# Optimization experiments

Hardware: AMD Instinct MI355X
Metric: run time of the kernel (lower is better)

## Reference

```python
import jax, jax.numpy as jnp
import numpy as np

N_GRAPHS = 20000
N_NODES = 7          # nodes per NAS cell
HID = 256            # hidden_dim
N_OPS = 5
TAU = 1.0


def _glorot(key, shape):
    s = 1.0 / np.sqrt(shape[0])
    return jax.random.normal(key, shape, jnp.float32) * s


def setup_inputs() -> dict:
    key = jax.random.key(0)
    ks = jax.random.split(key, 12)
    N = N_GRAPHS * N_NODES
    # fully-connected DAG edges inside each graph (upper triangular, 21 per graph)
    sl, dl = np.triu_indices(N_NODES, k=1)
    offs = (np.arange(N_GRAPHS) * N_NODES)[:, None]
    src = (offs + sl[None, :]).reshape(-1)
    dst = (offs + dl[None, :]).reshape(-1)
    edge_index = jnp.asarray(np.stack([src, dst]), dtype=jnp.int32)  # [2, E]
    batch = jnp.asarray(np.repeat(np.arange(N_GRAPHS), N_NODES), dtype=jnp.int32)
    E = edge_index.shape[1]
    return {
        "x": jax.random.normal(ks[0], (N, HID), jnp.float32),
        "edge_index": edge_index,
        "batch": batch,
        "W1": _glorot(ks[1], (HID, HID)), "b1": jnp.zeros((HID,), jnp.float32),
        "W2": _glorot(ks[2], (HID, HID)), "b2": jnp.zeros((HID,), jnp.float32),
        "We": _glorot(ks[3], (2 * HID, 2)), "be": jnp.zeros((2,), jnp.float32),
        "Wm": _glorot(ks[4], (HID, N_OPS)), "bm": jnp.zeros((N_OPS,), jnp.float32),
        "g_edge": jax.random.gumbel(ks[5], (E, 2), jnp.float32),
        "g_op": jax.random.gumbel(ks[6], (N, N_OPS), jnp.float32),
    }


def gcn_conv(x, edge_index, W, b, edge_weight=None):
    """PyG-style GCNConv: add self-loops (weight 1), symmetric normalization."""
    N = x.shape[0]
    src, dst = edge_index[0], edge_index[1]
    E = src.shape[0]
    ew = jnp.ones((E,), x.dtype) if edge_weight is None else edge_weight
    loop = jnp.arange(N, dtype=src.dtype)
    src_a = jnp.concatenate([src, loop])
    dst_a = jnp.concatenate([dst, loop])
    ew_a = jnp.concatenate([ew, jnp.ones((N,), x.dtype)])
    deg = jax.ops.segment_sum(ew_a, dst_a, num_segments=N)
    dinv = jnp.where(deg > 0, jax.lax.rsqrt(jnp.maximum(deg, 1e-12)), 0.0)
    norm = dinv[src_a] * ew_a * dinv[dst_a]  # [E+N]
    h = x @ W  # [N, out]
    msg = norm[:, None] * h[src_a]
    return jax.ops.segment_sum(msg, dst_a, num_segments=N) + b


def gumbel_softmax(logits, g, tau, hard):
    y = jax.nn.softmax((logits + g) / tau, axis=-1)
    if hard:
        y_hard = jax.nn.one_hot(jnp.argmax(y, axis=-1), y.shape[-1], dtype=y.dtype)
        y = y_hard + y - jax.lax.stop_gradient(y)
    return y


def reference(x, edge_index, batch, W1, b1, W2, b2, We, be, Wm, bm, g_edge, g_op):
    # mu=2 GCN layers with ReLU
    h = jax.nn.relu(gcn_conv(x, edge_index, W1, b1))
    h = jax.nn.relu(gcn_conv(h, edge_index, W2, b2))
    # edge scorer: 2-way gumbel-softmax over (keep, drop) per edge
    src, dst = edge_index[0], edge_index[1]
    pair = jnp.concatenate([h[src], h[dst]], axis=-1)  # [E, 2*HID]
    edge_logits = pair @ We + be                       # [E, 2]
    edges_scores = gumbel_softmax(edge_logits, g_edge, TAU, hard=False)
    # sample_pre=False branch: average the two score channels as edge weight
    avg_scores = (edges_scores[:, 0] + edges_scores[:, 1]) / 2
    op_emb = gcn_conv(h, edge_index, Wm, bm, edge_weight=avg_scores)  # [N, N_OPS]
    # hard straight-through gumbel-softmax over operations
    op_indices = gumbel_softmax(op_emb, g_op, TAU, hard=True)
    return op_indices
```

## Files before the change

kernel.cpp:

```cpp
#include <hip/hip_runtime.h>
#include <math.h>

#define HID 256

typedef __attribute__((ext_vector_type(8))) short v8s;
typedef __attribute__((ext_vector_type(4))) float v4f;

__device__ __forceinline__ float d1c(int i){ return 1.0f/sqrtf((float)(i+1)); }
__device__ __forceinline__ float d2c(int i){ return 1.0f/sqrtf(1.0f+0.5f*(float)i); }

__device__ __forceinline__ unsigned short f2bf(float x){
    unsigned u = __float_as_uint(x);
    u += 0x7fffu + ((u>>16)&1u);
    return (unsigned short)(u>>16);
}
__device__ __forceinline__ float bf2f(unsigned short b){
    return __uint_as_float(((unsigned)b)<<16);
}

__device__ __forceinline__ void mixA1_2(float (&v)[7][2]) {
#pragma unroll
    for (int r = 6; r >= 0; --r) {
        float t0 = 0.f, t1 = 0.f;
#pragma unroll
        for (int i = 0; i <= r; ++i) {
            const float c = d1c(i) * d1c(r);
            t0 = fmaf(c, v[i][0], t0);
            t1 = fmaf(c, v[i][1], t1);
        }
        v[r][0] = t0; v[r][1] = t1;
    }
}

__global__ void prep_w(const float* __restrict__ W1, const float* __restrict__ W2,
                       unsigned short* __restrict__ outw)
{
    const int tid = blockIdx.x*256 + threadIdx.x;
    if (tid >= 2*3*8*16*64) return;
    const int l  = tid & 63;
    const int c  = tid >> 6;
    const int nt = c & 15;
    const int k0 = (c>>4) & 7;
    const int s  = (c>>7) % 3;
    const int L  = c / (3*8*16);
    const float* W = L ? W2 : W1;
    const int n = nt*16 + (l & 15);
    unsigned short* o = outw + (size_t)tid*8;
#pragma unroll
    for (int e = 0; e < 8; ++e){
        const int k = k0*32 + (l>>4)*8 + e;
        float x = W[k*HID + n];
        unsigned short b0 = f2bf(x); float rr = x - bf2f(b0);
        unsigned short b1 = f2bf(rr); rr -= bf2f(b1);
        unsigned short b2 = f2bf(rr);
        o[e] = (s==0)? b0 : (s==1)? b1 : b2;
    }
}

__global__ __launch_bounds__(256, 2)
void nas_mfma(const float* __restrict__ X,
              const float* __restrict__ b1, const float* __restrict__ b2,
              const float* __restrict__ Wm, const float* __restrict__ bm,
              const float* __restrict__ g_op,
              const unsigned short* __restrict__ Bw,
              float* __restrict__ out)
{
    __shared__ __align__(16) char smem[49152];
    char*  Q0  = smem;
    char*  Q1  = smem + 24576;
    float* bq0 = (float*)smem;
    float* bq1 = (float*)(smem + 24576);
    float* bnc = (float*)smem;

    const int t   = threadIdx.x;
    const int w   = t >> 6;
    const int l   = t & 63;
    const int l15 = l & 15;
    const int q   = l >> 4;
    const int g   = t >> 5;
    const int t31 = t & 31;
    const long node0 = (long)blockIdx.x * 56;

    auto ws_q = [&](const float (&v)[7][2], char* qb){
        const int slotbase = t31 >> 2;
        const int byteoff  = (t31 & 3) * 4;
#pragma unroll
        for (int r = 0; r < 7; ++r){
            const int row  = g*7 + r;
            const int slot = slotbase ^ (row & 7);
            char* p = qb + row*128 + slot*16 + byteoff;
            unsigned h0[2], h1[2], h2[2];
#pragma unroll
            for (int j = 0; j < 2; ++j){
                float x = v[r][j];
                unsigned short a = f2bf(x); float rr = x - bf2f(a);
                unsigned short b = f2bf(rr); rr -= bf2f(b);
                unsigned short c = f2bf(rr);
                h0[j] = a; h1[j] = b; h2[j] = c;
            }
            *(unsigned*)(p)         = h0[0] | (h0[1] << 16);
            *(unsigned*)(p + 8192)  = h1[0] | (h1[1] << 16);
            *(unsigned*)(p + 16384) = h2[0] | (h2[1] << 16);
        }
    };

    auto gemm_q = [&](v4f (&ac)[4][4], const unsigned short* lbase, int qi,
                      const char* qb){
        const unsigned short* bbase = lbase + (size_t)w*512 + (size_t)l*8;
        v8s Bb[3][4];
        auto loadB = [&](int gi, int buf){
            const int ksl = gi/3, s2 = gi%3;
            const unsigned short* bp = bbase + (size_t)((s2*8 + qi*2 + ksl)*16)*512;
            Bb[buf][0] = *(const v8s*)(bp);
            Bb[buf][1] = *(const v8s*)(bp + 2048);
            Bb[buf][2] = *(const v8s*)(bp + 4096);
            Bb[buf][3] = *(const v8s*)(bp + 6144);
        };
        loadB(0, 0);
        loadB(1, 1);
        v8s A[3][4];
#pragma unroll
        for (int gi = 0; gi < 6; ++gi){
            const int ksl = gi/3, s2 = gi%3;
            if (s2 == 0){
                const int xorslot = ((ksl*4 + q) ^ (l15 & 7)) << 4;
#pragma unroll
                for (int s = 0; s < 3; ++s)
#pragma unroll
                for (int mt = 0; mt < 4; ++mt)
                    A[s][mt] = *(const v8s*)(qb + s*8192 + (mt*16 + l15)*128 + xorslot);
            }
            if (gi + 2 < 6) loadB(gi + 2, (gi + 2) % 3);
            const int buf = gi % 3;
            __builtin_amdgcn_s_setprio(1);
#pragma unroll
            for (int s1 = 0; s1 < 3; ++s1){
                if (s1 + s2 > 2) continue;
#pragma unroll
                for (int mt = 0; mt < 4; ++mt){
                    ac[mt][0] = __builtin_amdgcn_mfma_f32_16x16x32_bf16(A[s1][mt], Bb[buf][0], ac[mt][0],0,0,0);
                    ac[mt][1] = __builtin_amdgcn_mfma_f32_16x16x32_bf16(A[s1][mt], Bb[buf][1], ac[mt][1],0,0,0);
                    ac[mt][2] = __builtin_amdgcn_mfma_f32_16x16x32_bf16(A[s1][mt], Bb[buf][2], ac[mt][2],0,0,0);
                    ac[mt][3] = __builtin_amdgcn_mfma_f32_16x16x32_bf16(A[s1][mt], Bb[buf][3], ac[mt][3],0,0,0);
                }
            }
            __builtin_amdgcn_s_setprio(0);
        }
    };

    auto bw_q = [&](const v4f (&ac)[4][4], int p, float* bq){
        const int cc = (w*16 + l15) ^ (q << 4);
#pragma unroll
        for (int mt = 0; mt < 4; ++mt)
#pragma unroll
        for (int j = 0; j < 4; ++j)
            bq[(mt*16 + q*4 + j)*64 + cc] = ac[mt][p][j];
    };
    auto rd_q = [&](float (&v)[7][2], const float* bq){
#pragma unroll
        for (int r = 0; r < 7; ++r){
            const int row = g*7 + r;
            const int sw  = ((row >> 2) & 3) << 4;
            float2 f = *(const float2*)(&bq[row*64 + ((2*t31) ^ sw)]);
            v[r][0] = f.x; v[r][1] = f.y;
        }
    };
    auto brm = [&](float (&v)[7][2], const float* bias, int p){
        float2 bb = *(const float2*)(bias + p*64 + 2*t31);
#pragma unroll
        for (int r = 0; r < 7; ++r){
            v[r][0] = fmaxf(v[r][0] + bb.x, 0.0f);
            v[r][1] = fmaxf(v[r][1] + bb.y, 0.0f);
        }
        mixA1_2(v);
    };

    v4f acc[4][4];
#pragma unroll
    for (int mt=0;mt<4;++mt)
#pragma unroll
    for (int p=0;p<4;++p) acc[mt][p] = (v4f){0.f,0.f,0.f,0.f};

    float xq[4][7][2];
    {
        const float* xp = X + (node0 + g*7)*HID + 2*t31;
#pragma unroll
        for (int r = 0; r < 7; ++r)
#pragma unroll
        for (int qq = 0; qq < 4; ++qq){
            float2 f = *(const float2*)(xp + (long)r*HID + qq*64);
            xq[qq][r][0] = f.x; xq[qq][r][1] = f.y;
        }
#pragma unroll
        for (int qq = 0; qq < 4; ++qq) mixA1_2(xq[qq]);
    }

    ws_q(xq[0], Q0);
    __syncthreads();
    ws_q(xq[1], Q1); gemm_q(acc, Bw, 0, Q0);
    __syncthreads();
    ws_q(xq[2], Q0); gemm_q(acc, Bw, 1, Q1);
    __syncthreads();
    ws_q(xq[3], Q1); gemm_q(acc, Bw, 2, Q0);
    __syncthreads();
    gemm_q(acc, Bw, 3, Q1); bw_q(acc, 0, bq0);
    __syncthreads();

    v4f acc2[4][4];
#pragma unroll
    for (int mt=0;mt<4;++mt)
#pragma unroll
    for (int p=0;p<4;++p) acc2[mt][p] = (v4f){0.f,0.f,0.f,0.f};
    const unsigned short* Bw2 = Bw + 196608;

    float v0[7][2], v1[7][2];
    rd_q(v0, bq0); bw_q(acc, 1, bq1);
    __syncthreads();
    brm(v0, b1, 0); ws_q(v0, Q0); rd_q(v1, bq1);
    __syncthreads();
    brm(v1, b1, 1); ws_q(v1, Q1); gemm_q(acc2, Bw2, 0, Q0);
    __syncthreads();
    bw_q(acc, 2, bq0); gemm_q(acc2, Bw2, 1, Q1);
    __syncthreads();
    rd_q(v0, bq0); bw_q(acc, 3, bq1);
    __syncthreads();
    brm(v0, b1, 2); ws_q(v0, Q0); rd_q(v1, bq1);
    __syncthreads();
    brm(v1, b1, 3); ws_q(v1, Q1); gemm_q(acc2, Bw2, 2, Q0);
    __syncthreads();
    gemm_q(acc2, Bw2, 3, Q1);
    __syncthreads();

    auto bw2 = [&](const v4f (&ac)[4][4], int h){
#pragma unroll
        for (int pb = 0; pb < 2; ++pb){
            const int p  = 2*h + pb;
            const int lc = (w + 4*pb)*16 + l15;
            const int sw = ((q&1)<<4) ^ ((q>>1)<<2);
#pragma unroll
            for (int mt = 0; mt < 4; ++mt)
#pragma unroll
            for (int j = 0; j < 4; ++j){
                const int row = mt*16 + q*4 + j;
                bnc[row*128 + (lc ^ sw)] = ac[mt][p][j];
            }
        }
    };

    float pm[7][5];
#pragma unroll
    for (int r=0;r<7;++r)
#pragma unroll
    for (int p=0;p<5;++p) pm[r][p] = 0.0f;

    auto stage_pm = [&](int h){
        float v[7][4];
        const int lc = 4*t31;
#pragma unroll
        for (int r = 0; r < 7; ++r){
            const int row = g*7 + r;
            const int qq  = (row>>2)&3;
            const int sw  = ((qq&1)<<4) ^ ((qq>>1)<<2);
            float4 f = *(const float4*)(&bnc[row*128 + (lc ^ sw)]);
            v[r][0]=f.x; v[r][1]=f.y; v[r][2]=f.z; v[r][3]=f.w;
        }
        float4 bb = *(const float4*)(b2 + h*128 + 4*t31);
        const float bia[4] = {bb.x, bb.y, bb.z, bb.w};
#pragma unroll
        for (int r = 0; r < 7; ++r)
#pragma unroll
        for (int j = 0; j < 4; ++j)
            v[r][j] = fmaxf(v[r][j] + bia[j], 0.0f);
        const int colg = h*128 + 4*t31;
#pragma unroll
        for (int j = 0; j < 4; ++j){
            const float* wr = Wm + (colg + j)*5;
            float w5[5];
#pragma unroll
            for (int p = 0; p < 5; ++p) w5[p] = wr[p];
#pragma unroll
            for (int r = 0; r < 7; ++r)
#pragma unroll
            for (int p = 0; p < 5; ++p)
                pm[r][p] = fmaf(v[r][j], w5[p], pm[r][p]);
        }
    };

    bw2(acc2, 0);
    __syncthreads();
    stage_pm(0);
    __syncthreads();
    bw2(acc2, 1);
    __syncthreads();
    stage_pm(1);

#pragma unroll
    for (int m = 16; m >= 1; m >>= 1)
#pragma unroll
        for (int r = 0; r < 7; ++r)
#pragma unroll
            for (int p = 0; p < 5; ++p)
                pm[r][p] += __shfl_xor(pm[r][p], m, 64);

    if (t31 < 7){
        const int rr = t31;
        const long node = node0 + g*7 + rr;
        const float d2r = d2c(rr);
        float op[5];
#pragma unroll
        for (int p = 0; p < 5; ++p) op[p] = bm[p];
#pragma unroll
        for (int i = 0; i < 7; ++i){
            const float wgt = (i > rr) ? 0.0f
                            : (((i < rr) ? 0.5f : 1.0f) * d2c(i) * d2r);
#pragma unroll
            for (int p = 0; p < 5; ++p)
                op[p] = fmaf(wgt, pm[i][p], op[p]);
        }
        const float* gp = g_op + node*5;
        float best = op[0] + gp[0];
        int bi = 0;
#pragma unroll
        for (int p = 1; p < 5; ++p){
            float u = op[p] + gp[p];
            if (u > best) { best = u; bi = p; }
        }
        float* o = out + node*5;
#pragma unroll
        for (int p = 0; p < 5; ++p) o[p] = (p == bi) ? 1.0f : 0.0f;
    }
}

extern "C" void kernel_launch(void* const* d_in, const int* in_sizes, int n_in,
                              void* d_out, int out_size, void* d_ws, size_t ws_size,
                              hipStream_t stream)
{
    const float* X   = (const float*)d_in[0];
    const float* W1  = (const float*)d_in[3];
    const float* b1  = (const float*)d_in[4];
    const float* W2  = (const float*)d_in[5];
    const float* b2  = (const float*)d_in[6];
    const float* Wm  = (const float*)d_in[9];
    const float* bm  = (const float*)d_in[10];
    const float* gop = (const float*)d_in[12];
    float* out = (float*)d_out;

    unsigned short* wsplit = (unsigned short*)d_ws;

    prep_w<<<192, 256, 0, stream>>>(W1, W2, wsplit);

    const int N       = in_sizes[0] / HID;
    const int ngraph  = N / 7;
    const int nblocks = ngraph / 8;

    nas_mfma<<<nblocks, 256, 0, stream>>>(X, b1, b2, Wm, bm, gop, wsplit, out);
}
```

Before: 403.9 us.

## Halve per-block tile to 4 graphs to raise occupancy and cut registers

```diff
diff --git a/kernel.cpp b/kernel.cpp
--- a/kernel.cpp
+++ b/kernel.cpp
@@ -16,20 +16,6 @@
 }
 __device__ __forceinline__ float bf2f(unsigned short b){
     return __uint_as_float(((unsigned)b)<<16);
-}
-
-__device__ __forceinline__ void mixA1_2(float (&v)[7][2]) {
-#pragma unroll
-    for (int r = 6; r >= 0; --r) {
-        float t0 = 0.f, t1 = 0.f;
-#pragma unroll
-        for (int i = 0; i <= r; ++i) {
-            const float c = d1c(i) * d1c(r);
-            t0 = fmaf(c, v[i][0], t0);
-            t1 = fmaf(c, v[i][1], t1);
-        }
-        v[r][0] = t0; v[r][1] = t1;
-    }
 }
 
 __global__ void prep_w(const float* __restrict__ W1, const float* __restrict__ W2,
@@ -57,7 +43,7 @@
     }
 }
 
-__global__ __launch_bounds__(256, 2)
+__global__ __launch_bounds__(256, 3)
 void nas_mfma(const float* __restrict__ X,
               const float* __restrict__ b1, const float* __restrict__ b2,
               const float* __restrict__ Wm, const float* __restrict__ bm,
@@ -65,49 +51,41 @@
               const unsigned short* __restrict__ Bw,
               float* __restrict__ out)
 {
-    __shared__ __align__(16) char smem[49152];
+    __shared__ __align__(16) char smem[24576];
     char*  Q0  = smem;
-    char*  Q1  = smem + 24576;
+    char*  Q1  = smem + 12288;
     float* bq0 = (float*)smem;
-    float* bq1 = (float*)(smem + 24576);
-    float* bnc = (float*)smem;
+    float* bq1 = (float*)(smem + 12288);
 
     const int t   = threadIdx.x;
     const int w   = t >> 6;
     const int l   = t & 63;
     const int l15 = l & 15;
     const int q   = l >> 4;
-    const int g   = t >> 5;
-    const int t31 = t & 31;
-    const long node0 = (long)blockIdx.x * 56;
-
-    auto ws_q = [&](const float (&v)[7][2], char* qb){
-        const int slotbase = t31 >> 2;
-        const int byteoff  = (t31 & 3) * 4;
+    const long node0 = (long)blockIdx.x * 28;
+
+    auto ws_q = [&](const float (&v)[7], char* qb){
+        const int slotpre = l >> 3;
+        const int byteoff = (l & 7) * 2;
 #pragma unroll
         for (int r = 0; r < 7; ++r){
-            const int row  = g*7 + r;
-            const int slot = slotbase ^ (row & 7);
+            const int row  = w*7 + r;
+            const int slot = slotpre ^ (row & 7);
             char* p = qb + row*128 + slot*16 + byteoff;
-            unsigned h0[2], h1[2], h2[2];
-#pragma unroll
-            for (int j = 0; j < 2; ++j){
-                float x = v[r][j];
-                unsigned short a = f2bf(x); float rr = x - bf2f(a);
-                unsigned short b = f2bf(rr); rr -= bf2f(b);
-                unsigned short c = f2bf(rr);
-                h0[j] = a; h1[j] = b; h2[j] = c;
-            }
-            *(unsigned*)(p)         = h0[0] | (h0[1] << 16);
-            *(unsigned*)(p + 8192)  = h1[0] | (h1[1] << 16);
-            *(unsigned*)(p + 16384) = h2[0] | (h2[1] << 16);
-        }
-    };
-
-    auto gemm_q = [&](v4f (&ac)[4][4], const unsigned short* lbase, int qi,
+            float x = v[r];
+            unsigned short a = f2bf(x); float rr = x - bf2f(a);
+            unsigned short b = f2bf(rr); rr -= bf2f(b);
+            unsigned short c = f2bf(rr);
+            *(unsigned short*)(p)        = a;
+            *(unsigned short*)(p + 4096) = b;
+            *(unsigned short*)(p + 8192) = c;
+        }
+    };
+
+    auto gemm_q = [&](v4f (&ac)[2][4], const unsigned short* lbase, int qi,
                       const char* qb){
         const unsigned short* bbase = lbase + (size_t)w*512 + (size_t)l*8;
-        v8s Bb[3][4];
+        v8s Bb[2][4];
         auto loadB = [&](int gi, int buf){
             const int ksl = gi/3, s2 = gi%3;
             const unsigned short* bp = bbase + (size_t)((s2*8 + qi*2 + ksl)*16)*512;
@@ -117,8 +95,7 @@
             Bb[buf][3] = *(const v8s*)(bp + 6144);
         };
         loadB(0, 0);
-        loadB(1, 1);
-        v8s A[3][4];
+        v8s A[3][2];
 #pragma unroll
         for (int gi = 0; gi < 6; ++gi){
             const int ksl = gi/3, s2 = gi%3;
@@ -127,17 +104,17 @@
 #pragma unroll
                 for (int s = 0; s < 3; ++s)
 #pragma unroll
-                for (int mt = 0; mt < 4; ++mt)
-                    A[s][mt] = *(const v8s*)(qb + s*8192 + (mt*16 + l15)*128 + xorslot);
+                for (int mt = 0; mt < 2; ++mt)
+                    A[s][mt] = *(const v8s*)(qb + s*4096 + (mt*16 + l15)*128 + xorslot);
             }
-            if (gi + 2 < 6) loadB(gi + 2, (gi + 2) % 3);
-            const int buf = gi % 3;
+            if (gi + 1 < 6) loadB(gi + 1, (gi + 1) & 1);
+            const int buf = gi & 1;
             __builtin_amdgcn_s_setprio(1);
 #pragma unroll
             for (int s1 = 0; s1 < 3; ++s1){
                 if (s1 + s2 > 2) continue;
 #pragma unroll
-                for (int mt = 0; mt < 4; ++mt){
+                for (int mt = 0; mt < 2; ++mt){
                     ac[mt][0] = __builtin_amdgcn_mfma_f32_16x16x32_bf16(A[s1][mt], Bb[buf][0], ac[mt][0],0,0,0);
                     ac[mt][1] = __builtin_amdgcn_mfma_f32_16x16x32_bf16(A[s1][mt], Bb[buf][1], ac[mt][1],0,0,0);
                     ac[mt][2] = __builtin_amdgcn_mfma_f32_16x16x32_bf16(A[s1][mt], Bb[buf][2], ac[mt][2],0,0,0);
@@ -148,104 +125,85 @@
         }
     };
 
-    auto bw_q = [&](const v4f (&ac)[4][4], int p, float* bq){
+    auto bw_q = [&](const v4f (&ac)[2][4], int p, float* bq){
         const int cc = (w*16 + l15) ^ (q << 4);
 #pragma unroll
-        for (int mt = 0; mt < 4; ++mt)
+        for (int mt = 0; mt < 2; ++mt)
 #pragma unroll
         for (int j = 0; j < 4; ++j)
             bq[(mt*16 + q*4 + j)*64 + cc] = ac[mt][p][j];
     };
-    auto rd_q = [&](float (&v)[7][2], const float* bq){
+    auto rd_s = [&](float (&v)[7], const float* bq){
 #pragma unroll
         for (int r = 0; r < 7; ++r){
-            const int row = g*7 + r;
+            const int row = w*7 + r;
             const int sw  = ((row >> 2) & 3) << 4;
-            float2 f = *(const float2*)(&bq[row*64 + ((2*t31) ^ sw)]);
-            v[r][0] = f.x; v[r][1] = f.y;
-        }
-    };
-    auto brm = [&](float (&v)[7][2], const float* bias, int p){
-        float2 bb = *(const float2*)(bias + p*64 + 2*t31);
-#pragma unroll
-        for (int r = 0; r < 7; ++r){
-            v[r][0] = fmaxf(v[r][0] + bb.x, 0.0f);
-            v[r][1] = fmaxf(v[r][1] + bb.y, 0.0f);
-        }
-        mixA1_2(v);
-    };
-
-    v4f acc[4][4];
-#pragma unroll
-    for (int mt=0;mt<4;++mt)
+            v[r] = bq[row*64 + (l ^ sw)];
+        }
+    };
+    auto mix7 = [&](float (&v)[7]){
+#pragma unroll
+        for (int r = 6; r >= 0; --r){
+            float tt = 0.f;
+#pragma unroll
+            for (int i = 0; i <= r; ++i) tt = fmaf(d1c(i)*d1c(r), v[i], tt);
+            v[r] = tt;
+        }
+    };
+    auto brm = [&](float (&v)[7], const float* bias, int p){
+        const float bb = bias[p*64 + l];
+#pragma unroll
+        for (int r = 0; r < 7; ++r) v[r] = fmaxf(v[r] + bb, 0.0f);
+        mix7(v);
+    };
+    auto ldx = [&](float (&v)[7], int qq){
+        const float* xp = X + (node0 + w*7)*HID + qq*64 + l;
+#pragma unroll
+        for (int r = 0; r < 7; ++r) v[r] = xp[(long)r*HID];
+    };
+
+    v4f acc[2][4];
+#pragma unroll
+    for (int mt=0;mt<2;++mt)
 #pragma unroll
     for (int p=0;p<4;++p) acc[mt][p] = (v4f){0.f,0.f,0.f,0.f};
 
-    float xq[4][7][2];
-    {
-        const float* xp = X + (node0 + g*7)*HID + 2*t31;
-#pragma unroll
-        for (int r = 0; r < 7; ++r)
-#pragma unroll
-        for (int qq = 0; qq < 4; ++qq){
-            float2 f = *(const float2*)(xp + (long)r*HID + qq*64);
-            xq[qq][r][0] = f.x; xq[qq][r][1] = f.y;
-        }
-#pragma unroll
-        for (int qq = 0; qq < 4; ++qq) mixA1_2(xq[qq]);
-    }
-
-    ws_q(xq[0], Q0);
-    __syncthreads();
-    ws_q(xq[1], Q1); gemm_q(acc, Bw, 0, Q0);
-    __syncthreads();
-    ws_q(xq[2], Q0); gemm_q(acc, Bw, 1, Q1);
-    __syncthreads();
-    ws_q(xq[3], Q1); gemm_q(acc, Bw, 2, Q0);
+    float va[7], vb[7];
+    ldx(va, 0); mix7(va); ws_q(va, Q0);
+    ldx(vb, 1); mix7(vb);
+    __syncthreads();
+    ws_q(vb, Q1); ldx(va, 2); mix7(va); gemm_q(acc, Bw, 0, Q0);
+    __syncthreads();
+    ws_q(va, Q0); ldx(vb, 3); mix7(vb); gemm_q(acc, Bw, 1, Q1);
+    __syncthreads();
+    ws_q(vb, Q1); gemm_q(acc, Bw, 2, Q0);
     __syncthreads();
     gemm_q(acc, Bw, 3, Q1); bw_q(acc, 0, bq0);
     __syncthreads();
 
-    v4f acc2[4][4];
-#pragma unroll
-    for (int mt=0;mt<4;++mt)
+    v4f acc2[2][4];
+#pragma unroll
+    for (int mt=0;mt<2;++mt)
 #pragma unroll
     for (int p=0;p<4;++p) acc2[mt][p] = (v4f){0.f,0.f,0.f,0.f};
     const unsigned short* Bw2 = Bw + 196608;
 
-    float v0[7][2], v1[7][2];
-    rd_q(v0, bq0); bw_q(acc, 1, bq1);
-    __syncthreads();
-    brm(v0, b1, 0); ws_q(v0, Q0); rd_q(v1, bq1);
-    __syncthreads();
-    brm(v1, b1, 1); ws_q(v1, Q1); gemm_q(acc2, Bw2, 0, Q0);
+    rd_s(va, bq0); bw_q(acc, 1, bq1);
+    __syncthreads();
+    brm(va, b1, 0); ws_q(va, Q0); rd_s(vb, bq1);
+    __syncthreads();
+    brm(vb, b1, 1); ws_q(vb, Q1); gemm_q(acc2, Bw2, 0, Q0);
     __syncthreads();
     bw_q(acc, 2, bq0); gemm_q(acc2, Bw2, 1, Q1);
     __syncthreads();
-    rd_q(v0, bq0); bw_q(acc, 3, bq1);
-    __syncthreads();
-    brm(v0, b1, 2); ws_q(v0, Q0); rd_q(v1, bq1);
-    __syncthreads();
-    brm(v1, b1, 3); ws_q(v1, Q1); gemm_q(acc2, Bw2, 2, Q0);
-    __syncthreads();
-    gemm_q(acc2, Bw2, 3, Q1);
-    __syncthreads();
-
-    auto bw2 = [&](const v4f (&ac)[4][4], int h){
-#pragma unroll
-        for (int pb = 0; pb < 2; ++pb){
-            const int p  = 2*h + pb;
-            const int lc = (w + 4*pb)*16 + l15;
-            const int sw = ((q&1)<<4) ^ ((q>>1)<<2);
-#pragma unroll
-            for (int mt = 0; mt < 4; ++mt)
-#pragma unroll
-            for (int j = 0; j < 4; ++j){
-                const int row = mt*16 + q*4 + j;
-                bnc[row*128 + (lc ^ sw)] = ac[mt][p][j];
-            }
-        }
-    };
+    rd_s(va, bq0); bw_q(acc, 3, bq1);
+    __syncthreads();
+    brm(va, b1, 2); ws_q(va, Q0); rd_s(vb, bq1);
+    __syncthreads();
+    brm(vb, b1, 3); ws_q(vb, Q1); gemm_q(acc2, Bw2, 2, Q0);
+    __syncthreads();
+    gemm_q(acc2, Bw2, 3, Q1); bw_q(acc2, 0, bq0);
+    __syncthreads();
 
     float pm[7][5];
 #pragma unroll
@@ -253,58 +211,42 @@
 #pragma unroll
     for (int p=0;p<5;++p) pm[r][p] = 0.0f;
 
-    auto stage_pm = [&](int h){
-        float v[7][4];
-        const int lc = 4*t31;
-#pragma unroll
-        for (int r = 0; r < 7; ++r){
-            const int row = g*7 + r;
-            const int qq  = (row>>2)&3;
-            const int sw  = ((qq&1)<<4) ^ ((qq>>1)<<2);
-            float4 f = *(const float4*)(&bnc[row*128 + (lc ^ sw)]);
-            v[r][0]=f.x; v[r][1]=f.y; v[r][2]=f.z; v[r][3]=f.w;
-        }
-        float4 bb = *(const float4*)(b2 + h*128 + 4*t31);
-        const float bia[4] = {bb.x, bb.y, bb.z, bb.w};
+    auto pm_q = [&](int p, const float* bq){
+        float v[7];
+        rd_s(v, bq);
+        const float bb = b2[p*64 + l];
+#pragma unroll
+        for (int r = 0; r < 7; ++r) v[r] = fmaxf(v[r] + bb, 0.0f);
+        const float* wr = Wm + (p*64 + l)*5;
+        float w5[5];
+#pragma unroll
+        for (int j = 0; j < 5; ++j) w5[j] = wr[j];
 #pragma unroll
         for (int r = 0; r < 7; ++r)
 #pragma unroll
-        for (int j = 0; j < 4; ++j)
-            v[r][j] = fmaxf(v[r][j] + bia[j], 0.0f);
-        const int colg = h*128 + 4*t31;
-#pragma unroll
-        for (int j = 0; j < 4; ++j){
-            const float* wr = Wm + (colg + j)*5;
-            float w5[5];
-#pragma unroll
-            for (int p = 0; p < 5; ++p) w5[p] = wr[p];
-#pragma unroll
-            for (int r = 0; r < 7; ++r)
-#pragma unroll
-            for (int p = 0; p < 5; ++p)
-                pm[r][p] = fmaf(v[r][j], w5[p], pm[r][p]);
-        }
-    };
-
-    bw2(acc2, 0);
-    __syncthreads();
-    stage_pm(0);
-    __syncthreads();
-    bw2(acc2, 1);
-    __syncthreads();
-    stage_pm(1);
-
-#pragma unroll
-    for (int m = 16; m >= 1; m >>= 1)
+        for (int j = 0; j < 5; ++j)
+            pm[r][j] = fmaf(v[r], w5[j], pm[r][j]);
+    };
+
+    pm_q(0, bq0); bw_q(acc2, 1, bq1);
+    __syncthreads();
+    pm_q(1, bq1); bw_q(acc2, 2, bq0);
+    __syncthreads();
+    pm_q(2, bq0); bw_q(acc2, 3, bq1);
+    __syncthreads();
+    pm_q(3, bq1);
+
+#pragma unroll
+    for (int m = 32; m >= 1; m >>= 1)
 #pragma unroll
         for (int r = 0; r < 7; ++r)
 #pragma unroll
             for (int p = 0; p < 5; ++p)
                 pm[r][p] += __shfl_xor(pm[r][p], m, 64);
 
-    if (t31 < 7){
-        const int rr = t31;
-        const long node = node0 + g*7 + rr;
+    if (l < 7){
+        const int rr = l;
+        const long node = node0 + w*7 + rr;
         const float d2r = d2c(rr);
         float op[5];
 #pragma unroll
@@ -351,7 +293,6 @@
 
     const int N       = in_sizes[0] / HID;
     const int ngraph  = N / 7;
-    const int nblocks = ngraph / 8;
-
+    const int nblocks = ngraph / 4;
     nas_mfma<<<nblocks, 256, 0, stream>>>(X, b1, b2, Wm, bm, gop, wsplit, out);
 }
```

Measured after the change: 421.4 us. 4.3% more time.

## Single-buffer LDS staging and cut registers to fit three blocks per CU

Applied to the files above, without the earlier changes.

```diff
diff --git a/kernel.cpp b/kernel.cpp
--- a/kernel.cpp
+++ b/kernel.cpp
@@ -57,7 +57,7 @@
     }
 }
 
-__global__ __launch_bounds__(256, 2)
+__global__ __launch_bounds__(256, 3)
 void nas_mfma(const float* __restrict__ X,
               const float* __restrict__ b1, const float* __restrict__ b2,
               const float* __restrict__ Wm, const float* __restrict__ bm,
@@ -65,12 +65,9 @@
               const unsigned short* __restrict__ Bw,
               float* __restrict__ out)
 {
-    __shared__ __align__(16) char smem[49152];
-    char*  Q0  = smem;
-    char*  Q1  = smem + 24576;
-    float* bq0 = (float*)smem;
-    float* bq1 = (float*)(smem + 24576);
-    float* bnc = (float*)smem;
+    __shared__ __align__(16) char smem[24576 + 16384];
+    char*  Q  = smem;
+    float* bq = (float*)(smem + 24576);
 
     const int t   = threadIdx.x;
     const int w   = t >> 6;
@@ -81,33 +78,35 @@
     const int t31 = t & 31;
     const long node0 = (long)blockIdx.x * 56;
 
-    auto ws_q = [&](const float (&v)[7][2], char* qb){
-        const int slotbase = t31 >> 2;
-        const int byteoff  = (t31 & 3) * 4;
+    auto split2 = [&](float x, float y, unsigned &u0, unsigned &u1, unsigned &u2){
+        asm("v_cvt_pk_bf16_f32 %0, %1, %2" : "=v"(u0) : "v"(x), "v"(y));
+        float rx = x - __uint_as_float(u0 << 16);
+        float ry = y - __uint_as_float(u0 & 0xffff0000u);
+        asm("v_cvt_pk_bf16_f32 %0, %1, %2" : "=v"(u1) : "v"(rx), "v"(ry));
+        rx -= __uint_as_float(u1 << 16);
+        ry -= __uint_as_float(u1 & 0xffff0000u);
+        asm("v_cvt_pk_bf16_f32 %0, %1, %2" : "=v"(u2) : "v"(rx), "v"(ry));
+    };
+
+    auto ws_q = [&](const float (&v)[7][2]){
+        const int hs      = t31 >> 2;
+        const int byteoff = (t31 & 3) * 4;
 #pragma unroll
         for (int r = 0; r < 7; ++r){
             const int row  = g*7 + r;
-            const int slot = slotbase ^ (row & 7);
-            char* p = qb + row*128 + slot*16 + byteoff;
-            unsigned h0[2], h1[2], h2[2];
-#pragma unroll
-            for (int j = 0; j < 2; ++j){
-                float x = v[r][j];
-                unsigned short a = f2bf(x); float rr = x - bf2f(a);
-                unsigned short b = f2bf(rr); rr -= bf2f(b);
-                unsigned short c = f2bf(rr);
-                h0[j] = a; h1[j] = b; h2[j] = c;
-            }
-            *(unsigned*)(p)         = h0[0] | (h0[1] << 16);
-            *(unsigned*)(p + 8192)  = h1[0] | (h1[1] << 16);
-            *(unsigned*)(p + 16384) = h2[0] | (h2[1] << 16);
-        }
-    };
-
-    auto gemm_q = [&](v4f (&ac)[4][4], const unsigned short* lbase, int qi,
-                      const char* qb){
+            const int slot = hs ^ (row & 7);
+            char* p = Q + row*128 + slot*16 + byteoff;
+            unsigned u0, u1, u2;
+            split2(v[r][0], v[r][1], u0, u1, u2);
+            *(unsigned*)(p)         = u0;
+            *(unsigned*)(p + 8192)  = u1;
+            *(unsigned*)(p + 16384) = u2;
+        }
+    };
+
+    auto gemm_q = [&](v4f (&ac)[4][4], const unsigned short* lbase, int qi){
         const unsigned short* bbase = lbase + (size_t)w*512 + (size_t)l*8;
-        v8s Bb[3][4];
+        v8s Bb[2][4];
         auto loadB = [&](int gi, int buf){
             const int ksl = gi/3, s2 = gi%3;
             const unsigned short* bp = bbase + (size_t)((s2*8 + qi*2 + ksl)*16)*512;
@@ -117,21 +116,20 @@
             Bb[buf][3] = *(const v8s*)(bp + 6144);
         };
         loadB(0, 0);
-        loadB(1, 1);
         v8s A[3][4];
 #pragma unroll
         for (int gi = 0; gi < 6; ++gi){
             const int ksl = gi/3, s2 = gi%3;
             if (s2 == 0){
-                const int xorslot = ((ksl*4 + q) ^ (l15 & 7)) << 4;
+                const int xorslot = ((ksl*4 + q) ^ (l & 7)) << 4;
 #pragma unroll
                 for (int s = 0; s < 3; ++s)
 #pragma unroll
                 for (int mt = 0; mt < 4; ++mt)
-                    A[s][mt] = *(const v8s*)(qb + s*8192 + (mt*16 + l15)*128 + xorslot);
+                    A[s][mt] = *(const v8s*)(Q + s*8192 + (mt*16 + l15)*128 + xorslot);
             }
-            if (gi + 2 < 6) loadB(gi + 2, (gi + 2) % 3);
-            const int buf = gi % 3;
+            if (gi + 1 < 6) loadB(gi + 1, (gi + 1) & 1);
+            const int buf = gi & 1;
             __builtin_amdgcn_s_setprio(1);
 #pragma unroll
             for (int s1 = 0; s1 < 3; ++s1){
@@ -148,7 +146,7 @@
         }
     };
 
-    auto bw_q = [&](const v4f (&ac)[4][4], int p, float* bq){
+    auto bw_q = [&](const v4f (&ac)[4][4], int p){
         const int cc = (w*16 + l15) ^ (q << 4);
 #pragma unroll
         for (int mt = 0; mt < 4; ++mt)
@@ -156,7 +154,7 @@
         for (int j = 0; j < 4; ++j)
             bq[(mt*16 + q*4 + j)*64 + cc] = ac[mt][p][j];
     };
-    auto rd_q = [&](float (&v)[7][2], const float* bq){
+    auto rd_q = [&](float (&v)[7][2]){
 #pragma unroll
         for (int r = 0; r < 7; ++r){
             const int row = g*7 + r;
@@ -174,6 +172,14 @@
         }
         mixA1_2(v);
     };
+    auto ldx = [&](float (&v)[7][2], int qq){
+        const float* xp = X + (node0 + g*7)*HID + qq*64 + 2*t31;
+#pragma unroll
+        for (int r = 0; r < 7; ++r){
+            float2 f = *(const float2*)(xp + (long)r*HID);
+            v[r][0] = f.x; v[r][1] = f.y;
+        }
+    };
 
     v4f acc[4][4];
 #pragma unroll
@@ -181,30 +187,16 @@
 #pragma unroll
     for (int p=0;p<4;++p) acc[mt][p] = (v4f){0.f,0.f,0.f,0.f};
 
-    float xq[4][7][2];
     {
-        const float* xp = X + (node0 + g*7)*HID + 2*t31;
-#pragma unroll
-        for (int r = 0; r < 7; ++r)
+        float v[7][2];
 #pragma unroll
         for (int qq = 0; qq < 4; ++qq){
-            float2 f = *(const float2*)(xp + (long)r*HID + qq*64);
-            xq[qq][r][0] = f.x; xq[qq][r][1] = f.y;
-        }
-#pragma unroll
-        for (int qq = 0; qq < 4; ++qq) mixA1_2(xq[qq]);
-    }
-
-    ws_q(xq[0], Q0);
-    __syncthreads();
-    ws_q(xq[1], Q1); gemm_q(acc, Bw, 0, Q0);
-    __syncthreads();
-    ws_q(xq[2], Q0); gemm_q(acc, Bw, 1, Q1);
-    __syncthreads();
-    ws_q(xq[3], Q1); gemm_q(acc, Bw, 2, Q0);
-    __syncthreads();
-    gemm_q(acc, Bw, 3, Q1); bw_q(acc, 0, bq0);
-    __syncthreads();
+            if (qq) __syncthreads();
+            ldx(v, qq); mixA1_2(v); ws_q(v);
+            __syncthreads();
+            gemm_q(acc, Bw, qq);
+        }
+    }
 
     v4f acc2[4][4];
 #pragma unroll
@@ -213,86 +205,54 @@
     for (int p=0;p<4;++p) acc2[mt][p] = (v4f){0.f,0.f,0.f,0.f};
     const unsigned short* Bw2 = Bw + 196608;
 
-    float v0[7][2], v1[7][2];
-    rd_q(v0, bq0); bw_q(acc, 1, bq1);
+    bw_q(acc, 0);
     __syncthreads();
-    brm(v0, b1, 0); ws_q(v0, Q0); rd_q(v1, bq1);
-    __syncthreads();
-    brm(v1, b1, 1); ws_q(v1, Q1); gemm_q(acc2, Bw2, 0, Q0);
-    __syncthreads();
-    bw_q(acc, 2, bq0); gemm_q(acc2, Bw2, 1, Q1);
-    __syncthreads();
-    rd_q(v0, bq0); bw_q(acc, 3, bq1);
-    __syncthreads();
-    brm(v0, b1, 2); ws_q(v0, Q0); rd_q(v1, bq1);
-    __syncthreads();
-    brm(v1, b1, 3); ws_q(v1, Q1); gemm_q(acc2, Bw2, 2, Q0);
-    __syncthreads();
-    gemm_q(acc2, Bw2, 3, Q1);
-    __syncthreads();
-
-    auto bw2 = [&](const v4f (&ac)[4][4], int h){
-#pragma unroll
-        for (int pb = 0; pb < 2; ++pb){
-            const int p  = 2*h + pb;
-            const int lc = (w + 4*pb)*16 + l15;
-            const int sw = ((q&1)<<4) ^ ((q>>1)<<2);
-#pragma unroll
-            for (int mt = 0; mt < 4; ++mt)
-#pragma unroll
-            for (int j = 0; j < 4; ++j){
-                const int row = mt*16 + q*4 + j;
-                bnc[row*128 + (lc ^ sw)] = ac[mt][p][j];
+    {
+        float v[7][2];
+#pragma unroll
+        for (int p = 0; p < 4; ++p){
+            rd_q(v); brm(v, b1, p); ws_q(v);
+            __syncthreads();
+            if (p < 3) bw_q(acc, p + 1);
+            gemm_q(acc2, Bw2, p);
+            __syncthreads();
+        }
+    }
+
+    float pm[7][5];
+#pragma unroll
+    for (int r=0;r<7;++r)
+#pragma unroll
+    for (int p=0;p<5;++p) pm[r][p] = 0.0f;
+
+#pragma unroll
+    for (int p = 0; p < 4; ++p){
+        bw_q(acc2, p);
+        __syncthreads();
+        {
+            float v[7][2];
+            rd_q(v);
+            float2 bb = *(const float2*)(b2 + p*64 + 2*t31);
+#pragma unroll
+            for (int r = 0; r < 7; ++r){
+                v[r][0] = fmaxf(v[r][0] + bb.x, 0.0f);
+                v[r][1] = fmaxf(v[r][1] + bb.y, 0.0f);
             }
-        }
-    };
-
-    float pm[7][5];
-#pragma unroll
-    for (int r=0;r<7;++r)
-#pragma unroll
-    for (int p=0;p<5;++p) pm[r][p] = 0.0f;
-
-    auto stage_pm = [&](int h){
-        float v[7][4];
-        const int lc = 4*t31;
-#pragma unroll
-        for (int r = 0; r < 7; ++r){
-            const int row = g*7 + r;
-            const int qq  = (row>>2)&3;
-            const int sw  = ((qq&1)<<4) ^ ((qq>>1)<<2);
-            float4 f = *(const float4*)(&bnc[row*128 + (lc ^ sw)]);
-            v[r][0]=f.x; v[r][1]=f.y; v[r][2]=f.z; v[r][3]=f.w;
-        }
-        float4 bb = *(const float4*)(b2 + h*128 + 4*t31);
-        const float bia[4] = {bb.x, bb.y, bb.z, bb.w};
-#pragma unroll
-        for (int r = 0; r < 7; ++r)
-#pragma unroll
-        for (int j = 0; j < 4; ++j)
-            v[r][j] = fmaxf(v[r][j] + bia[j], 0.0f);
-        const int colg = h*128 + 4*t31;
-#pragma unroll
-        for (int j = 0; j < 4; ++j){
-            const float* wr = Wm + (colg + j)*5;
-            float w5[5];
-#pragma unroll
-            for (int p = 0; p < 5; ++p) w5[p] = wr[p];
-#pragma unroll
-            for (int r = 0; r < 7; ++r)
-#pragma unroll
-            for (int p = 0; p < 5; ++p)
-                pm[r][p] = fmaf(v[r][j], w5[p], pm[r][p]);
-        }
-    };
-
-    bw2(acc2, 0);
-    __syncthreads();
-    stage_pm(0);
-    __syncthreads();
-    bw2(acc2, 1);
-    __syncthreads();
-    stage_pm(1);
+#pragma unroll
+            for (int j = 0; j < 2; ++j){
+                const float* wr = Wm + (p*64 + 2*t31 + j)*5;
+                float w5[5];
+#pragma unroll
+                for (int pp = 0; pp < 5; ++pp) w5[pp] = wr[pp];
+#pragma unroll
+                for (int r = 0; r < 7; ++r)
+#pragma unroll
+                for (int pp = 0; pp < 5; ++pp)
+                    pm[r][pp] = fmaf(v[r][j], w5[pp], pm[r][pp]);
+            }
+        }
+        if (p < 3) __syncthreads();
+    }
 
 #pragma unroll
     for (int m = 16; m >= 1; m >>= 1)
@@ -352,6 +312,5 @@
     const int N       = in_sizes[0] / HID;
     const int ngraph  = N / 7;
     const int nblocks = ngraph / 8;
-
     nas_mfma<<<nblocks, 256, 0, stream>>>(X, b1, b2, Wm, bm, gop, wsplit, out);
 }
```

After: 385.7 us. 1.05x faster.
